# Optimization experiments

Measured on AMD Instinct MI355X. Metric: run time of the kernel, lower is better.

## Reference

```python
import jax, jax.numpy as jnp
import numpy as np

HIDDEN = 1024
HEADS = 16
HEAD_DIM = HIDDEN // HEADS
GAMMA = 0.5
B, S = 2, 2048


def setup_inputs() -> dict:
    key = jax.random.key(0)
    ks = jax.random.split(key, 9)
    sc = 1.0 / np.sqrt(HIDDEN)
    x = jax.random.normal(ks[0], (B, S, HIDDEN), dtype=jnp.float32)
    attn_mask = jnp.zeros((S, S), dtype=bool)  # True = masked; all-False here
    Wq = jax.random.normal(ks[1], (HIDDEN, HIDDEN), dtype=jnp.float32) * sc
    bq = jnp.zeros((HIDDEN,), dtype=jnp.float32)
    Wk = jax.random.normal(ks[2], (HIDDEN, HIDDEN), dtype=jnp.float32) * sc
    bk = jnp.zeros((HIDDEN,), dtype=jnp.float32)
    Wv = jax.random.normal(ks[3], (HIDDEN, HIDDEN), dtype=jnp.float32) * sc
    bv = jnp.zeros((HIDDEN,), dtype=jnp.float32)
    Wo = jax.random.normal(ks[4], (HIDDEN, HIDDEN), dtype=jnp.float32) * sc
    bo = jnp.zeros((HIDDEN,), dtype=jnp.float32)
    return {"x": x, "attn_mask": attn_mask, "Wq": Wq, "bq": bq,
            "Wk": Wk, "bk": bk, "Wv": Wv, "bv": bv, "Wo": Wo, "bo": bo}


def reference(x, attn_mask, Wq, bq, Wk, bk, Wv, bv, Wo, bo):
    Bn, Sn, _ = x.shape
    # projections (torch Linear: x @ W.T + b), reshape to [B, H, S, Dh]
    def proj(W, b):
        y = x @ W.T + b
        return y.reshape(Bn, Sn, HEADS, HEAD_DIM).transpose(0, 2, 1, 3)
    q, k, v = proj(Wq, bq), proj(Wk, bk), proj(Wv, bv)
    scores = jnp.einsum('bhqd,bhkd->bhqk', q, k) / np.sqrt(HEAD_DIM)
    # diversity bias: cosine similarity of raw x (F.normalize eps=1e-12)
    normed = x / jnp.maximum(jnp.linalg.norm(x, axis=-1, keepdims=True), 1e-12)
    sim = jnp.einsum('bqd,bkd->bqk', normed, normed)
    scores = scores - GAMMA * sim[:, None, :, :]
    scores = jnp.where(attn_mask[None, None, :, :], -jnp.inf, scores)
    probs = jax.nn.softmax(scores, axis=-1)
    ctx = jnp.einsum('bhqk,bhkd->bhqd', probs, v)
    ctx = ctx.transpose(0, 2, 1, 3).reshape(Bn, Sn, HIDDEN)
    return ctx @ Wo.T + bo
```

## Files before the change

### kernel.cpp

```cpp
#include <hip/hip_runtime.h>

#define HID 1024
#define SEQ 2048
#define NB 2
#define NH 16
#define HD 64

#define C1 0.1803368801111204f
#define C2 0.7213475204444817f

typedef __attribute__((ext_vector_type(8))) short bf16x8;
typedef __attribute__((ext_vector_type(8))) unsigned short u16x8;
typedef __attribute__((ext_vector_type(4))) float f32x4;

__device__ __forceinline__ unsigned short f2bf(float f) {
  unsigned u = __builtin_bit_cast(unsigned, f);
  u += 0x7fffu + ((u >> 16) & 1u);
  return (unsigned short)(u >> 16);
}
__device__ __forceinline__ float bf2f(unsigned short u) {
  return __builtin_bit_cast(float, ((unsigned)u) << 16);
}

#define GLOAD16(gsrc, ldst)                                                     \
  __builtin_amdgcn_global_load_lds(                                             \
      (const __attribute__((address_space(1))) void*)(gsrc),                    \
      (__attribute__((address_space(3))) void*)(ldst), 16, 0, 0)

__global__ __launch_bounds__(256) void convert_w_kernel(
    const float* __restrict__ Wq, const float* __restrict__ Wk,
    const float* __restrict__ Wv, const float* __restrict__ Wo,
    unsigned short* __restrict__ Wb) {
  int i = blockIdx.x * 256 + threadIdx.x;
  const int per = (HID * HID) / 8;
  int m = i / per;
  const float* sp = (m == 0) ? Wq : (m == 1) ? Wk : (m == 2) ? Wv : Wo;
  int j = (i - m * per) * 8;
  const float4* p = reinterpret_cast<const float4*>(sp + j);
  float4 a = p[0], b = p[1];
  u16x8 o;
  o[0] = f2bf(a.x); o[1] = f2bf(a.y); o[2] = f2bf(a.z); o[3] = f2bf(a.w);
  o[4] = f2bf(b.x); o[5] = f2bf(b.y); o[6] = f2bf(b.z); o[7] = f2bf(b.w);
  *reinterpret_cast<u16x8*>(Wb + (size_t)i * 8) = o;
}

__global__ __launch_bounds__(256) void rownorm_kernel(
    const float* __restrict__ x, unsigned short* __restrict__ xb,
    unsigned short* __restrict__ nxb) {
  int row = blockIdx.x, tid = threadIdx.x;
  const float4 v = reinterpret_cast<const float4*>(x + (size_t)row * HID)[tid];
  float ss = v.x * v.x + v.y * v.y + v.z * v.z + v.w * v.w;
#pragma unroll
  for (int off = 32; off; off >>= 1) ss += __shfl_xor(ss, off, 64);
  __shared__ float wsum[4];
  if ((tid & 63) == 0) wsum[tid >> 6] = ss;
  __syncthreads();
  float tot = wsum[0] + wsum[1] + wsum[2] + wsum[3];
  float inv = 1.0f / fmaxf(sqrtf(tot), 1e-12f);
  ushort4 a, b;
  a.x = f2bf(v.x); a.y = f2bf(v.y); a.z = f2bf(v.z); a.w = f2bf(v.w);
  b.x = f2bf(v.x * inv); b.y = f2bf(v.y * inv);
  b.z = f2bf(v.z * inv); b.w = f2bf(v.w * inv);
  reinterpret_cast<ushort4*>(xb  + (size_t)row * HID)[tid] = a;
  reinterpret_cast<ushort4*>(nxb + (size_t)row * HID)[tid] = b;
}

template <int MODE>
__global__ __launch_bounds__(256) void gemm_nt(
    const unsigned short* __restrict__ A, long strideA,
    const unsigned short* __restrict__ B, long strideB,
    void* __restrict__ Cv, long strideC, int ldc,
    int M, int N, int K,
    const float* __restrict__ b0, const float* __restrict__ b1,
    const float* __restrict__ b2, const unsigned char* __restrict__ mask) {
  __shared__ __align__(16) unsigned short As[128 * 32];
  __shared__ __align__(16) unsigned short Bs[128 * 32];
  int tid = threadIdx.x, lane = tid & 63, wid = tid >> 6;
  int g = lane >> 4, lr = lane & 15;
  int wr = wid >> 1, wc = wid & 1;
  int m0 = blockIdx.y * 128, n0 = blockIdx.x * 128;
  const unsigned short* Ab = A + (size_t)blockIdx.z * strideA
      + (size_t)(m0 + wid * 32 + (lane >> 2)) * K + (lane & 3) * 8;
  const unsigned short* Bb = B + (size_t)blockIdx.z * strideB
      + (size_t)(n0 + wid * 32 + (lane >> 2)) * K + (lane & 3) * 8;
  unsigned short* la = As + wid * 1024;
  unsigned short* lb = Bs + wid * 1024;
  f32x4 acc[4][4] = {};
  for (int k0 = 0; k0 < K; k0 += 32) {
    GLOAD16(Ab + k0, la);
    GLOAD16(Ab + 16 * K + k0, la + 512);
    GLOAD16(Bb + k0, lb);
    GLOAD16(Bb + 16 * K + k0, lb + 512);
    __syncthreads();
    bf16x8 af[4], bfr[4];
#pragma unroll
    for (int i = 0; i < 4; i++) {
      af[i]  = *reinterpret_cast<const bf16x8*>(&As[(wr * 64 + i * 16 + lr) * 32 + g * 8]);
      bfr[i] = *reinterpret_cast<const bf16x8*>(&Bs[(wc * 64 + i * 16 + lr) * 32 + g * 8]);
    }
#pragma unroll
    for (int i = 0; i < 4; i++)
#pragma unroll
      for (int j = 0; j < 4; j++)
        acc[i][j] = __builtin_amdgcn_mfma_f32_16x16x32_bf16(af[i], bfr[j], acc[i][j], 0, 0, 0);
    __syncthreads();
  }
#pragma unroll
  for (int i = 0; i < 4; i++)
#pragma unroll
    for (int j = 0; j < 4; j++) {
      int col = n0 + wc * 64 + j * 16 + lr;
#pragma unroll
      for (int r = 0; r < 4; r++) {
        int row = m0 + wr * 64 + i * 16 + 4 * g + r;
        float v = acc[i][j][r];
        if (MODE == 0) {
          const float* bp = (col < 1024) ? b0 : (col < 2048 ? b1 : b2);
          v += bp[col & 1023];
          ((unsigned short*)Cv)[(size_t)blockIdx.z * strideC + (size_t)row * ldc + col] = f2bf(v);
        } else if (MODE == 1) {
          float t = -C2 * v + (mask[(size_t)row * N + col] ? -1e30f : 0.0f);
          ((unsigned short*)Cv)[(size_t)blockIdx.z * strideC + (size_t)row * ldc + col] = f2bf(t);
        } else {
          v += b0[col];
          ((float*)Cv)[(size_t)blockIdx.z * strideC + (size_t)row * ldc + col] = v;
        }
      }
    }
}

__global__ __launch_bounds__(256, 4) void flash_kernel(
    const unsigned short* __restrict__ QKV,
    const unsigned short* __restrict__ D2,
    unsigned short* __restrict__ ctxb) {
  int h = blockIdx.x, qt = blockIdx.y, b = blockIdx.z;
  int tid = threadIdx.x, wid = tid >> 6, lane = tid & 63;
  int g = lane >> 4, lr = lane & 15;
  __shared__ __align__(16) unsigned short Ks[2][64 * 64];
  __shared__ __align__(16) unsigned short Vt[2][64 * 64];
  __shared__ __align__(16) unsigned short Pl[4][16 * 64];
  const size_t ld = 3 * HID;
  const size_t bS = (size_t)b * SEQ;
  const int qbase = qt * 64 + wid * 16;

  const unsigned short* qp = QKV + (bS + qbase + lr) * ld + h * HD + g * 8;
  bf16x8 qf0 = *reinterpret_cast<const bf16x8*>(qp);
  bf16x8 qf1 = *reinterpret_cast<const bf16x8*>(qp + 32);

  const unsigned short* gK0 = QKV + (bS + wid * 16 + (lane >> 3)) * ld + HID + h * HD
                              + (((lane & 7) ^ (lane >> 3)) << 3);
  const unsigned short* gK1 = gK0 + 8 * ld;

  const int vr0 = tid >> 3, ch = tid & 7;
  const unsigned short* gV0 = QKV + (bS + vr0) * ld + 2 * HID + h * HD + (ch << 3);
  const unsigned short* gV1 = gV0 + 32 * ld;
  const int kr3 = vr0 & 7;
  const int kb0v = vr0 >> 3, kb1v = kb0v + 4;
  const int vtbase = ch * 512 + kr3;
  const int pre0 = (kb0v ^ ch) & 7, pre1 = (kb1v ^ ch) & 7;

  const unsigned short* bD = D2 + (size_t)b * SEQ * SEQ
                             + (size_t)(qbase + lr) * SEQ + 4 * g;

  GLOAD16(gK0, &Ks[0][wid * 1024]);
  GLOAD16(gK1, &Ks[0][wid * 1024 + 512]);
  {
    u16x8 v0 = *reinterpret_cast<const u16x8*>(gV0);
    u16x8 v1 = *reinterpret_cast<const u16x8*>(gV1);
#pragma unroll
    for (int i = 0; i < 8; i++) {
      Vt[0][vtbase + i * 64 + ((pre0 ^ i) << 3)] = v0[i];
      Vt[0][vtbase + i * 64 + ((pre1 ^ i) << 3)] = v1[i];
    }
  }
  ushort4 bvc[4];
#pragma unroll
  for (int kc = 0; kc < 4; kc++)
    bvc[kc] = *reinterpret_cast<const ushort4*>(bD + kc * 16);
  __syncthreads();

  f32x4 acc[4] = {};
  f32x4 rsacc = {};
  const int kb0 = lr * 64 + ((g ^ (lr & 7)) << 3);
  const int plw = lr * 64;
  const int plm = (lr & 7) << 3;
  bf16x8 ones;
#pragma unroll
  for (int i = 0; i < 8; i++) ones[i] = 0x3F80;

  for (int kt = 0; kt < 32; ++kt) {
    const int cb = kt & 1;
    const unsigned short* ks = &Ks[cb][0];
    const unsigned short* vt = &Vt[cb][0];
    u16x8 vv0 = {}, vv1 = {};
    ushort4 bvn[4];
    if (kt < 31) {
      GLOAD16(gK0 + (size_t)(kt + 1) * 64 * ld, &Ks[cb ^ 1][wid * 1024]);
      GLOAD16(gK1 + (size_t)(kt + 1) * 64 * ld, &Ks[cb ^ 1][wid * 1024 + 512]);
      vv0 = *reinterpret_cast<const u16x8*>(gV0 + (size_t)(kt + 1) * 64 * ld);
      vv1 = *reinterpret_cast<const u16x8*>(gV1 + (size_t)(kt + 1) * 64 * ld);
#pragma unroll
      for (int kc = 0; kc < 4; kc++)
        bvn[kc] = *reinterpret_cast<const ushort4*>(bD + (kt + 1) * 64 + kc * 16);
    }

    f32x4 s[4];
    __builtin_amdgcn_s_setprio(1);
#pragma unroll
    for (int kc = 0; kc < 4; kc++) {
      bf16x8 kf0 = *reinterpret_cast<const bf16x8*>(ks + kc * 1024 + kb0);
      bf16x8 kf1 = *reinterpret_cast<const bf16x8*>(ks + kc * 1024 + (kb0 ^ 32));
      f32x4 z = {};
      z = __builtin_amdgcn_mfma_f32_16x16x32_bf16(kf0, qf0, z, 0, 0, 0);
      s[kc] = __builtin_amdgcn_mfma_f32_16x16x32_bf16(kf1, qf1, z, 0, 0, 0);
    }
    __builtin_amdgcn_s_setprio(0);

#pragma unroll
    for (int kc = 0; kc < 4; kc++) {
      float p0 = exp2f(fmaf(s[kc][0], C1, bf2f(bvc[kc].x)));
      float p1 = exp2f(fmaf(s[kc][1], C1, bf2f(bvc[kc].y)));
      float p2 = exp2f(fmaf(s[kc][2], C1, bf2f(bvc[kc].z)));
      float p3 = exp2f(fmaf(s[kc][3], C1, bf2f(bvc[kc].w)));
      uint2 w;
      w.x = __builtin_amdgcn_perm(__builtin_bit_cast(unsigned, p1),
                                  __builtin_bit_cast(unsigned, p0), 0x07060302u);
      w.y = __builtin_amdgcn_perm(__builtin_bit_cast(unsigned, p3),
                                  __builtin_bit_cast(unsigned, p2), 0x07060302u);
      *reinterpret_cast<uint2*>(&Pl[wid][plw + ((kc * 16 + 4 * g) ^ plm)]) = w;
    }

    __builtin_amdgcn_s_setprio(1);
#pragma unroll
    for (int c2 = 0; c2 < 2; c2++) {
      bf16x8 pf = *reinterpret_cast<const bf16x8*>(
          &Pl[wid][plw + ((c2 * 32 + g * 8) ^ plm)]);
      rsacc = __builtin_amdgcn_mfma_f32_16x16x32_bf16(pf, ones, rsacc, 0, 0, 0);
#pragma unroll
      for (int df = 0; df < 4; df++) {
        int blk = ((4 * c2 + g) ^ (lr & 7) ^ ((df * 2 + (lr >> 3)) & 7)) & 7;
        bf16x8 vf = *reinterpret_cast<const bf16x8*>(vt + (df * 16 + lr) * 64 + (blk << 3));
        acc[df] = __builtin_amdgcn_mfma_f32_16x16x32_bf16(pf, vf, acc[df], 0, 0, 0);
      }
    }
    __builtin_amdgcn_s_setprio(0);

    if (kt < 31) {
#pragma unroll
      for (int i = 0; i < 8; i++) {
        Vt[cb ^ 1][vtbase + i * 64 + ((pre0 ^ i) << 3)] = vv0[i];
        Vt[cb ^ 1][vtbase + i * 64 + ((pre1 ^ i) << 3)] = vv1[i];
      }
      bvc[0] = bvn[0]; bvc[1] = bvn[1]; bvc[2] = bvn[2]; bvc[3] = bvn[3];
    }
    __syncthreads();
  }
  float l0 = 1.0f / rsacc[0], l1 = 1.0f / rsacc[1];
  float l2 = 1.0f / rsacc[2], l3 = 1.0f / rsacc[3];
  unsigned short* op = ctxb + (bS + qbase + 4 * g) * HID + h * HD + lr;
#pragma unroll
  for (int df = 0; df < 4; df++) {
    op[0 * HID + df * 16] = f2bf(acc[df][0] * l0);
    op[1 * HID + df * 16] = f2bf(acc[df][1] * l1);
    op[2 * HID + df * 16] = f2bf(acc[df][2] * l2);
    op[3 * HID + df * 16] = f2bf(acc[df][3] * l3);
  }
}

extern "C" void kernel_launch(void* const* d_in, const int* in_sizes, int n_in,
                              void* d_out, int out_size, void* d_ws, size_t ws_size,
                              hipStream_t stream) {
  const float* x = (const float*)d_in[0];
  const unsigned char* mask = (const unsigned char*)d_in[1];
  const float* Wq = (const float*)d_in[2];
  const float* bq = (const float*)d_in[3];
  const float* Wk = (const float*)d_in[4];
  const float* bk = (const float*)d_in[5];
  const float* Wv = (const float*)d_in[6];
  const float* bv = (const float*)d_in[7];
  const float* Wo = (const float*)d_in[8];
  const float* bo = (const float*)d_in[9];
  float* out = (float*)d_out;

  char* ws = (char*)d_ws;
  const size_t MiB = 1024 * 1024;
  unsigned short* xb  = (unsigned short*)(ws + 0 * MiB);
  unsigned short* nxb = (unsigned short*)(ws + 8 * MiB);
  unsigned short* Wb  = (unsigned short*)(ws + 16 * MiB);
  unsigned short* QKV = (unsigned short*)(ws + 24 * MiB);
  unsigned short* D2  = (unsigned short*)(ws + 48 * MiB);
  unsigned short* ctx = (unsigned short*)(ws + 64 * MiB);

  convert_w_kernel<<<2048, 256, 0, stream>>>(Wq, Wk, Wv, Wo, Wb);
  rownorm_kernel<<<NB * SEQ, 256, 0, stream>>>(x, xb, nxb);
  gemm_nt<0><<<dim3(24, 32, 1), 256, 0, stream>>>(
      xb, 0, Wb, 0, QKV, 0, 3 * HID, NB * SEQ, 3 * HID, HID, bq, bk, bv, nullptr);
  gemm_nt<1><<<dim3(16, 16, 2), 256, 0, stream>>>(
      nxb, (long)SEQ * HID, nxb, (long)SEQ * HID, D2, (long)SEQ * SEQ, SEQ,
      SEQ, SEQ, HID, nullptr, nullptr, nullptr, mask);
  flash_kernel<<<dim3(NH, SEQ / 64, NB), 256, 0, stream>>>(QKV, D2, ctx);
  gemm_nt<2><<<dim3(8, 32, 1), 256, 0, stream>>>(
      ctx, 0, Wb + (size_t)3 * HID * HID, 0, out, 0, HID, NB * SEQ, HID, HID,
      bo, nullptr, nullptr, nullptr);
}
```

Before: 215.2 us.

## Permute key rows so softmax probabilities feed PV MFMA directly from registers

Reorders which key rows are loaded into each K shared-memory slot, so the S=K·Q MFMA output layout lines up with the A-operand layout needed for the P·V MFMA. Probabilities are then packed into bf16x8 registers in place, with no round trip through the per-wave Pl shared buffer. The diagonal-bias loads are remapped to the new key order to match. This removes LDS writes and reads plus their latency from every key tile and frees shared memory. The cost is tricky index bookkeeping that has to stay consistent between the K permutation, the bias offsets and the V layout.

```diff
diff --git a/kernel.cpp b/kernel.cpp
--- a/kernel.cpp
+++ b/kernel.cpp
@@ -138,7 +138,6 @@
   int g = lane >> 4, lr = lane & 15;
   __shared__ __align__(16) unsigned short Ks[2][64 * 64];
   __shared__ __align__(16) unsigned short Vt[2][64 * 64];
-  __shared__ __align__(16) unsigned short Pl[4][16 * 64];
   const size_t ld = 3 * HID;
   const size_t bS = (size_t)b * SEQ;
   const int qbase = qt * 64 + wid * 16;
@@ -147,9 +146,12 @@
   bf16x8 qf0 = *reinterpret_cast<const bf16x8*>(qp);
   bf16x8 qf1 = *reinterpret_cast<const bf16x8*>(qp + 32);
 
-  const unsigned short* gK0 = QKV + (bS + wid * 16 + (lane >> 3)) * ld + HID + h * HD
+  const int p0 = wid * 16 + (lane >> 3);
+  const int key0 = ((p0 >> 5) & 1) * 32 + (((p0 >> 2) & 3) << 3)
+                 + ((p0 >> 4) & 1) * 4 + (p0 & 3);
+  const unsigned short* gK0 = QKV + (bS + key0) * ld + HID + h * HD
                               + (((lane & 7) ^ (lane >> 3)) << 3);
-  const unsigned short* gK1 = gK0 + 8 * ld;
+  const unsigned short* gK1 = gK0 + 16 * ld;
 
   const int vr0 = tid >> 3, ch = tid & 7;
   const unsigned short* gV0 = QKV + (bS + vr0) * ld + 2 * HID + h * HD + (ch << 3);
@@ -160,7 +162,7 @@
   const int pre0 = (kb0v ^ ch) & 7, pre1 = (kb1v ^ ch) & 7;
 
   const unsigned short* bD = D2 + (size_t)b * SEQ * SEQ
-                             + (size_t)(qbase + lr) * SEQ + 4 * g;
+                             + (size_t)(qbase + lr) * SEQ + 8 * g;
 
   GLOAD16(gK0, &Ks[0][wid * 1024]);
   GLOAD16(gK1, &Ks[0][wid * 1024 + 512]);
@@ -174,16 +176,15 @@
     }
   }
   ushort4 bvc[4];
-#pragma unroll
-  for (int kc = 0; kc < 4; kc++)
-    bvc[kc] = *reinterpret_cast<const ushort4*>(bD + kc * 16);
+  bvc[0] = *reinterpret_cast<const ushort4*>(bD + 0);
+  bvc[1] = *reinterpret_cast<const ushort4*>(bD + 4);
+  bvc[2] = *reinterpret_cast<const ushort4*>(bD + 32);
+  bvc[3] = *reinterpret_cast<const ushort4*>(bD + 36);
   __syncthreads();
 
   f32x4 acc[4] = {};
   f32x4 rsacc = {};
   const int kb0 = lr * 64 + ((g ^ (lr & 7)) << 3);
-  const int plw = lr * 64;
-  const int plm = (lr & 7) << 3;
   bf16x8 ones;
 #pragma unroll
   for (int i = 0; i < 8; i++) ones[i] = 0x3F80;
@@ -199,9 +200,11 @@
       GLOAD16(gK1 + (size_t)(kt + 1) * 64 * ld, &Ks[cb ^ 1][wid * 1024 + 512]);
       vv0 = *reinterpret_cast<const u16x8*>(gV0 + (size_t)(kt + 1) * 64 * ld);
       vv1 = *reinterpret_cast<const u16x8*>(gV1 + (size_t)(kt + 1) * 64 * ld);
-#pragma unroll
-      for (int kc = 0; kc < 4; kc++)
-        bvn[kc] = *reinterpret_cast<const ushort4*>(bD + (kt + 1) * 64 + kc * 16);
+      const unsigned short* bn = bD + (kt + 1) * 64;
+      bvn[0] = *reinterpret_cast<const ushort4*>(bn + 0);
+      bvn[1] = *reinterpret_cast<const ushort4*>(bn + 4);
+      bvn[2] = *reinterpret_cast<const ushort4*>(bn + 32);
+      bvn[3] = *reinterpret_cast<const ushort4*>(bn + 36);
     }
 
     f32x4 s[4];
@@ -216,31 +219,38 @@
     }
     __builtin_amdgcn_s_setprio(0);
 
-#pragma unroll
-    for (int kc = 0; kc < 4; kc++) {
-      float p0 = exp2f(fmaf(s[kc][0], C1, bf2f(bvc[kc].x)));
-      float p1 = exp2f(fmaf(s[kc][1], C1, bf2f(bvc[kc].y)));
-      float p2 = exp2f(fmaf(s[kc][2], C1, bf2f(bvc[kc].z)));
-      float p3 = exp2f(fmaf(s[kc][3], C1, bf2f(bvc[kc].w)));
-      uint2 w;
-      w.x = __builtin_amdgcn_perm(__builtin_bit_cast(unsigned, p1),
-                                  __builtin_bit_cast(unsigned, p0), 0x07060302u);
-      w.y = __builtin_amdgcn_perm(__builtin_bit_cast(unsigned, p3),
-                                  __builtin_bit_cast(unsigned, p2), 0x07060302u);
-      *reinterpret_cast<uint2*>(&Pl[wid][plw + ((kc * 16 + 4 * g) ^ plm)]) = w;
+    bf16x8 pa[2];
+#pragma unroll
+    for (int c2 = 0; c2 < 2; c2++) {
+      float p0f = exp2f(fmaf(s[2 * c2][0], C1, bf2f(bvc[2 * c2].x)));
+      float p1f = exp2f(fmaf(s[2 * c2][1], C1, bf2f(bvc[2 * c2].y)));
+      float p2f = exp2f(fmaf(s[2 * c2][2], C1, bf2f(bvc[2 * c2].z)));
+      float p3f = exp2f(fmaf(s[2 * c2][3], C1, bf2f(bvc[2 * c2].w)));
+      float p4f = exp2f(fmaf(s[2 * c2 + 1][0], C1, bf2f(bvc[2 * c2 + 1].x)));
+      float p5f = exp2f(fmaf(s[2 * c2 + 1][1], C1, bf2f(bvc[2 * c2 + 1].y)));
+      float p6f = exp2f(fmaf(s[2 * c2 + 1][2], C1, bf2f(bvc[2 * c2 + 1].z)));
+      float p7f = exp2f(fmaf(s[2 * c2 + 1][3], C1, bf2f(bvc[2 * c2 + 1].w)));
+      uint4 W;
+      W.x = __builtin_amdgcn_perm(__builtin_bit_cast(unsigned, p1f),
+                                  __builtin_bit_cast(unsigned, p0f), 0x07060302u);
+      W.y = __builtin_amdgcn_perm(__builtin_bit_cast(unsigned, p3f),
+                                  __builtin_bit_cast(unsigned, p2f), 0x07060302u);
+      W.z = __builtin_amdgcn_perm(__builtin_bit_cast(unsigned, p5f),
+                                  __builtin_bit_cast(unsigned, p4f), 0x07060302u);
+      W.w = __builtin_amdgcn_perm(__builtin_bit_cast(unsigned, p7f),
+                                  __builtin_bit_cast(unsigned, p6f), 0x07060302u);
+      pa[c2] = __builtin_bit_cast(bf16x8, W);
     }
 
     __builtin_amdgcn_s_setprio(1);
 #pragma unroll
     for (int c2 = 0; c2 < 2; c2++) {
-      bf16x8 pf = *reinterpret_cast<const bf16x8*>(
-          &Pl[wid][plw + ((c2 * 32 + g * 8) ^ plm)]);
-      rsacc = __builtin_amdgcn_mfma_f32_16x16x32_bf16(pf, ones, rsacc, 0, 0, 0);
+      rsacc = __builtin_amdgcn_mfma_f32_16x16x32_bf16(pa[c2], ones, rsacc, 0, 0, 0);
 #pragma unroll
       for (int df = 0; df < 4; df++) {
         int blk = ((4 * c2 + g) ^ (lr & 7) ^ ((df * 2 + (lr >> 3)) & 7)) & 7;
         bf16x8 vf = *reinterpret_cast<const bf16x8*>(vt + (df * 16 + lr) * 64 + (blk << 3));
-        acc[df] = __builtin_amdgcn_mfma_f32_16x16x32_bf16(pf, vf, acc[df], 0, 0, 0);
+        acc[df] = __builtin_amdgcn_mfma_f32_16x16x32_bf16(pa[c2], vf, acc[df], 0, 0, 0);
       }
     }
     __builtin_amdgcn_s_setprio(0);
```

Measured after the change: 194.5 us. 9.6% less time.
